# Kernel tuning notes

Measured on AMD Instinct MI355X. Metric: run time of the kernel, lower is better.

Reference implementation:

```python
import jax, jax.numpy as jnp
import numpy as np

N = 1_000_000
F_IN = 16
HID = 32
E = 16_000_000


def setup_inputs() -> dict:
    key = jax.random.key(0)
    ks = jax.random.split(key, 20)
    s = 0.1
    inp = {
        "x": jax.random.normal(ks[0], (N, F_IN), dtype=jnp.float32),
        "edge_index": jax.random.randint(ks[1], (2, E), 0, N, dtype=jnp.int64),
        "edge_weight": jax.random.uniform(ks[2], (E,), dtype=jnp.float32),
        # ChebConv(K=1) weights for the 3 GRU gates (x-side and h-side)
        "Wxz": jax.random.normal(ks[3], (F_IN, HID), dtype=jnp.float32) * s,
        "bxz": jnp.zeros((HID,), jnp.float32),
        "Whz": jax.random.normal(ks[4], (HID, HID), dtype=jnp.float32) * s,
        "bhz": jnp.zeros((HID,), jnp.float32),
        "Wxr": jax.random.normal(ks[5], (F_IN, HID), dtype=jnp.float32) * s,
        "bxr": jnp.zeros((HID,), jnp.float32),
        "Whr": jax.random.normal(ks[6], (HID, HID), dtype=jnp.float32) * s,
        "bhr": jnp.zeros((HID,), jnp.float32),
        "Wxh": jax.random.normal(ks[7], (F_IN, HID), dtype=jnp.float32) * s,
        "bxh": jnp.zeros((HID,), jnp.float32),
        "Whh": jax.random.normal(ks[8], (HID, HID), dtype=jnp.float32) * s,
        "bhh": jnp.zeros((HID,), jnp.float32),
        # final Linear(32, 1)
        "Wlin": jax.random.normal(ks[9], (HID, 1), dtype=jnp.float32) * s,
        "blin": jnp.zeros((1,), jnp.float32),
    }
    return inp


def _gconv_gru(x, Wxz, bxz, Whz, bhz, Wxr, bxr, Whr, bhr, Wxh, bxh, Whh, bhh):
    # GConvGRU with ChebConv K=1: each conv is T0(L)x @ W + b == x @ W + b
    # (edge_index / edge_weight are mathematically unused when K=1).
    H = jnp.zeros((x.shape[0], Whz.shape[0]), dtype=x.dtype)  # initial hidden state
    Z = jax.nn.sigmoid(x @ Wxz + bxz + H @ Whz + bhz)          # update gate
    R = jax.nn.sigmoid(x @ Wxr + bxr + H @ Whr + bhr)          # reset gate
    H_tilde = jnp.tanh(x @ Wxh + bxh + (R * H) @ Whh + bhh)    # candidate
    return Z * H + (1.0 - Z) * H_tilde


def reference(x, edge_index, edge_weight, Wxz, bxz, Whz, bhz, Wxr, bxr, Whr, bhr,
              Wxh, bxh, Whh, bhh, Wlin, blin):
    H = _gconv_gru(x, Wxz, bxz, Whz, bhz, Wxr, bxr, Whr, bhr, Wxh, bxh, Whh, bhh)
    h = jax.nn.relu(H)
    return h @ Wlin + blin  # [N, 1]
```

## Files before the change

### kernel.cpp

```cpp
#include <hip/hip_runtime.h>


constexpr int F = 16;
constexpr int HD = 32;

__global__ __launch_bounds__(256) void gconv_gru_fused(
    const float* __restrict__ x,
    const float* __restrict__ Wxz,
    const float* __restrict__ bxz,
    const float* __restrict__ bhz,
    const float* __restrict__ Wxh,
    const float* __restrict__ bxh,
    const float* __restrict__ bhh,
    const float* __restrict__ Wlin,
    const float* __restrict__ blin,
    float* __restrict__ out,
    int n)
{
    const int i = blockIdx.x * 256 + threadIdx.x;
    if (i >= n) return;

    const float4* xp = reinterpret_cast<const float4*>(x + (size_t)i * F);
    float xs[F];
    #pragma unroll
    for (int q = 0; q < 4; ++q) {
        float4 v = xp[q];
        xs[4 * q + 0] = v.x;
        xs[4 * q + 1] = v.y;
        xs[4 * q + 2] = v.z;
        xs[4 * q + 3] = v.w;
    }

    const float4* wz = reinterpret_cast<const float4*>(Wxz);
    const float4* wh = reinterpret_cast<const float4*>(Wxh);

    float accZ[HD];
    float accH[HD];
    #pragma unroll
    for (int j = 0; j < HD; ++j) { accZ[j] = 0.f; accH[j] = 0.f; }

    #pragma unroll
    for (int k = 0; k < F; ++k) {
        const float xk = xs[k];
        #pragma unroll
        for (int j4 = 0; j4 < HD / 4; ++j4) {
            const float4 w = wz[k * (HD / 4) + j4];
            accZ[4 * j4 + 0] = fmaf(xk, w.x, accZ[4 * j4 + 0]);
            accZ[4 * j4 + 1] = fmaf(xk, w.y, accZ[4 * j4 + 1]);
            accZ[4 * j4 + 2] = fmaf(xk, w.z, accZ[4 * j4 + 2]);
            accZ[4 * j4 + 3] = fmaf(xk, w.w, accZ[4 * j4 + 3]);
            const float4 v = wh[k * (HD / 4) + j4];
            accH[4 * j4 + 0] = fmaf(xk, v.x, accH[4 * j4 + 0]);
            accH[4 * j4 + 1] = fmaf(xk, v.y, accH[4 * j4 + 1]);
            accH[4 * j4 + 2] = fmaf(xk, v.z, accH[4 * j4 + 2]);
            accH[4 * j4 + 3] = fmaf(xk, v.w, accH[4 * j4 + 3]);
        }
    }

    float res = blin[0];
    #pragma unroll
    for (int j = 0; j < HD; ++j) {
        const float az = accZ[j] + bxz[j] + bhz[j];
        const float ah = accH[j] + bxh[j] + bhh[j];
        const float z = __builtin_amdgcn_rcpf(1.f + __expf(-az));
        const float th = 1.f - 2.f * __builtin_amdgcn_rcpf(1.f + __expf(2.f * ah));
        float hc = (1.f - z) * th;
        hc = fmaxf(hc, 0.f);
        res = fmaf(hc, Wlin[j], res);
    }
    out[i] = res;
}

extern "C" void kernel_launch(void* const* d_in, const int* in_sizes, int n_in,
                              void* d_out, int out_size, void* d_ws, size_t ws_size,
                              hipStream_t stream) {
    const float* x    = (const float*)d_in[0];
    const float* Wxz  = (const float*)d_in[3];
    const float* bxz  = (const float*)d_in[4];
    const float* bhz  = (const float*)d_in[6];
    const float* Wxh  = (const float*)d_in[11];
    const float* bxh  = (const float*)d_in[12];
    const float* bhh  = (const float*)d_in[14];
    const float* Wlin = (const float*)d_in[15];
    const float* blin = (const float*)d_in[16];
    float* out = (float*)d_out;

    const int n = in_sizes[0] / F;
    const int blocks = (n + 255) / 256;
    gconv_gru_fused<<<blocks, 256, 0, stream>>>(
        x, Wxz, bxz, bhz, Wxh, bxh, bhh, Wlin, blin, out, n);
}
```

Before: 275.6 us.

## Process four nodes per thread with packed FMA and merged gate transcendentals

Each thread now handles four nodes and holds two nodes per packed float2 register, so the 16x32 matmuls use packed fma and each weight load serves four nodes. The sigmoid and tanh are rewritten so that relu((1-z)*tanh) becomes max(e^{2a}-1,0)/((1+e^z)(1+e^{2a})), which needs one reciprocal instead of two. Hidden units are processed in chunks of four to keep register use bounded. The output is written with a float4 store. The launch assumes n is divisible by four, and the exponent is clamped to avoid overflow.

```diff
diff --git a/kernel.cpp b/kernel.cpp
--- a/kernel.cpp
+++ b/kernel.cpp
@@ -1,74 +1,107 @@
 #include <hip/hip_runtime.h>
 
 
-constexpr int F = 16;
-constexpr int HD = 32;
+typedef float v2f __attribute__((ext_vector_type(2)));
 
-__global__ __launch_bounds__(256) void gconv_gru_fused(
+constexpr int F   = 16;
+constexpr int HD  = 32;
+constexpr int NPT = 4;
+constexpr int JB  = 4;
+
+__global__ __launch_bounds__(256) void gru_fused(
     const float* __restrict__ x,
-    const float* __restrict__ Wxz,
-    const float* __restrict__ bxz,
+    const float* __restrict__ Wxz, const float* __restrict__ bxz,
     const float* __restrict__ bhz,
-    const float* __restrict__ Wxh,
-    const float* __restrict__ bxh,
+    const float* __restrict__ Wxh, const float* __restrict__ bxh,
     const float* __restrict__ bhh,
-    const float* __restrict__ Wlin,
-    const float* __restrict__ blin,
-    float* __restrict__ out,
-    int n)
+    const float* __restrict__ Wlin, const float* __restrict__ blin,
+    float* __restrict__ out, int n)
 {
-    const int i = blockIdx.x * 256 + threadIdx.x;
-    if (i >= n) return;
+    const int t = blockIdx.x * 256 + threadIdx.x;
+    const int base = t * NPT;
+    if (base >= n) return;
 
-    const float4* xp = reinterpret_cast<const float4*>(x + (size_t)i * F);
-    float xs[F];
+    float xs[NPT][F];
     #pragma unroll
-    for (int q = 0; q < 4; ++q) {
-        float4 v = xp[q];
-        xs[4 * q + 0] = v.x;
-        xs[4 * q + 1] = v.y;
-        xs[4 * q + 2] = v.z;
-        xs[4 * q + 3] = v.w;
-    }
-
-    const float4* wz = reinterpret_cast<const float4*>(Wxz);
-    const float4* wh = reinterpret_cast<const float4*>(Wxh);
-
-    float accZ[HD];
-    float accH[HD];
-    #pragma unroll
-    for (int j = 0; j < HD; ++j) { accZ[j] = 0.f; accH[j] = 0.f; }
-
-    #pragma unroll
-    for (int k = 0; k < F; ++k) {
-        const float xk = xs[k];
+    for (int m = 0; m < NPT; ++m) {
+        const float4* xp = reinterpret_cast<const float4*>(x + (size_t)(base + m) * F);
         #pragma unroll
-        for (int j4 = 0; j4 < HD / 4; ++j4) {
-            const float4 w = wz[k * (HD / 4) + j4];
-            accZ[4 * j4 + 0] = fmaf(xk, w.x, accZ[4 * j4 + 0]);
-            accZ[4 * j4 + 1] = fmaf(xk, w.y, accZ[4 * j4 + 1]);
-            accZ[4 * j4 + 2] = fmaf(xk, w.z, accZ[4 * j4 + 2]);
-            accZ[4 * j4 + 3] = fmaf(xk, w.w, accZ[4 * j4 + 3]);
-            const float4 v = wh[k * (HD / 4) + j4];
-            accH[4 * j4 + 0] = fmaf(xk, v.x, accH[4 * j4 + 0]);
-            accH[4 * j4 + 1] = fmaf(xk, v.y, accH[4 * j4 + 1]);
-            accH[4 * j4 + 2] = fmaf(xk, v.z, accH[4 * j4 + 2]);
-            accH[4 * j4 + 3] = fmaf(xk, v.w, accH[4 * j4 + 3]);
+        for (int q = 0; q < 4; ++q) {
+            float4 v = xp[q];
+            xs[m][4 * q + 0] = v.x;
+            xs[m][4 * q + 1] = v.y;
+            xs[m][4 * q + 2] = v.z;
+            xs[m][4 * q + 3] = v.w;
         }
     }
 
-    float res = blin[0];
+    float res[NPT];
     #pragma unroll
-    for (int j = 0; j < HD; ++j) {
-        const float az = accZ[j] + bxz[j] + bhz[j];
-        const float ah = accH[j] + bxh[j] + bhh[j];
-        const float z = __builtin_amdgcn_rcpf(1.f + __expf(-az));
-        const float th = 1.f - 2.f * __builtin_amdgcn_rcpf(1.f + __expf(2.f * ah));
-        float hc = (1.f - z) * th;
-        hc = fmaxf(hc, 0.f);
-        res = fmaf(hc, Wlin[j], res);
+    for (int m = 0; m < NPT; ++m) res[m] = blin[0];
+
+    #pragma unroll 1
+    for (int jb = 0; jb < HD / JB; ++jb) {
+        v2f accZ[JB][NPT / 2];
+        v2f accH[JB][NPT / 2];
+        #pragma unroll
+        for (int j = 0; j < JB; ++j) {
+            const int jj = jb * JB + j;
+            const float bz = bxz[jj] + bhz[jj];
+            const float bh = bxh[jj] + bhh[jj];
+            #pragma unroll
+            for (int p = 0; p < NPT / 2; ++p) {
+                v2f vz = {bz, bz};
+                v2f vh = {bh, bh};
+                accZ[j][p] = vz;
+                accH[j][p] = vh;
+            }
+        }
+
+        #pragma unroll
+        for (int k = 0; k < F; ++k) {
+            v2f xk[NPT / 2];
+            #pragma unroll
+            for (int p = 0; p < NPT / 2; ++p) {
+                v2f v = {xs[2 * p][k], xs[2 * p + 1][k]};
+                xk[p] = v;
+            }
+            #pragma unroll
+            for (int j = 0; j < JB; ++j) {
+                const int jj = jb * JB + j;
+                const float wz = Wxz[k * HD + jj];
+                const float wh = Wxh[k * HD + jj];
+                v2f wz2 = {wz, wz};
+                v2f wh2 = {wh, wh};
+                #pragma unroll
+                for (int p = 0; p < NPT / 2; ++p) {
+                    accZ[j][p] = __builtin_elementwise_fma(xk[p], wz2, accZ[j][p]);
+                    accH[j][p] = __builtin_elementwise_fma(xk[p], wh2, accH[j][p]);
+                }
+            }
+        }
+
+        #pragma unroll
+        for (int j = 0; j < JB; ++j) {
+            const int jj = jb * JB + j;
+            const float wl = Wlin[jj];
+            #pragma unroll
+            for (int p = 0; p < NPT / 2; ++p) {
+                #pragma unroll
+                for (int h = 0; h < 2; ++h) {
+                    const float az = accZ[j][p][h];
+                    const float ah = accH[j][p][h];
+                    const float u = __expf(az);
+                    const float v = __expf(fminf(2.f * ah, 87.f));
+                    const float r = __builtin_amdgcn_rcpf((1.f + u) * (1.f + v));
+                    const float num = fmaxf(v - 1.f, 0.f);
+                    res[2 * p + h] = fmaf(num * r, wl, res[2 * p + h]);
+                }
+            }
+        }
     }
-    out[i] = res;
+
+    float4 o = make_float4(res[0], res[1], res[2], res[3]);
+    *reinterpret_cast<float4*>(out + base) = o;
 }
 
 extern "C" void kernel_launch(void* const* d_in, const int* in_sizes, int n_in,
@@ -86,7 +119,8 @@
     float* out = (float*)d_out;
 
     const int n = in_sizes[0] / F;
-    const int blocks = (n + 255) / 256;
-    gconv_gru_fused<<<blocks, 256, 0, stream>>>(
+    const int threads = n / NPT;
+    const int blocks = (threads + 255) / 256;
+    gru_fused<<<blocks, 256, 0, stream>>>(
         x, Wxz, bxz, bhz, Wxh, bxh, bhh, Wlin, blin, out, n);
 }
```

After: 270.0 us. 1.02x faster.
